# Optimization experiments

Hardware: AMD Instinct MI355X
Metric: run time of the kernel (lower is better)

## Reference

```python
import jax, jax.numpy as jnp
import numpy as np

B, T, I, H, O = 64, 1024, 64, 512, 64


def setup_inputs() -> dict:
    key = jax.random.key(0)
    ks = jax.random.split(key, 8)
    s = 1.0 / np.sqrt(H)  # PyTorch nn.RNN / nn.Linear init scale
    u = lambda k, shape: jax.random.uniform(k, shape, jnp.float32, -s, s)
    return {
        "x": jax.random.normal(ks[0], (B, T, I), jnp.float32),
        "h": jnp.zeros((1, B, H), jnp.float32),
        "W_ih": u(ks[1], (H, I)),
        "W_hh": u(ks[2], (H, H)),
        "b_ih": u(ks[3], (H,)),
        "b_hh": u(ks[4], (H,)),
        "W_out": u(ks[5], (O, H)),
        "b_out": u(ks[6], (O,)),
    }


def reference(x, h, W_ih, W_hh, b_ih, b_hh, W_out, b_out):
    # Precompute input projection for all timesteps: [B, T, H]
    xp = jnp.einsum('bti,hi->bth', x, W_ih) + b_ih + b_hh

    def step(h_prev, xp_t):
        # h_t = tanh(x_t W_ih^T + b_ih + h_{t-1} W_hh^T + b_hh)
        h_t = jnp.tanh(xp_t + h_prev @ W_hh.T)
        return h_t, h_t

    h0 = h[0]  # [B, H]
    h_last, hs = jax.lax.scan(step, h0, jnp.swapaxes(xp, 0, 1))  # hs: [T, B, H]
    hs = jnp.swapaxes(hs, 0, 1)  # [B, T, H]
    out = jnp.tanh(jnp.einsum('bth,oh->bto', hs, W_out) + b_out)  # [B, T, O]
    return out, h_last[None]  # h returned as [1, B, H]
```

## Files before the change

### kernel.cpp

```cpp
#include <hip/hip_runtime.h>
#include <cstdint>
#include <cstddef>


#define BB 64
#define TT 1024
#define II 64
#define HH 512
#define OO 64

__device__ __forceinline__ float tanh_fast(float v) {
  float e = exp2f(fabsf(v) * 2.8853900817779268f);
  float r = 1.0f - 2.0f * __builtin_amdgcn_rcpf(e + 1.0f);
  return copysignf(r, v);
}

__global__ __launch_bounds__(512, 1) void rnn_persist(
    const float* __restrict__ x, const float* __restrict__ h0,
    const float* __restrict__ Wih, const float* __restrict__ Whh,
    const float* __restrict__ bih, const float* __restrict__ bhh,
    const float* __restrict__ Wout, const float* __restrict__ bout,
    float* __restrict__ out, unsigned long long* __restrict__ ring) {
  const int tid = threadIdx.x;
  const int b   = blockIdx.x & 63;
  const int q   = blockIdx.x >> 6;
  const int n   = tid >> 2;
  const int q4  = tid & 3;
  const int row = q * 128 + n;

  __shared__ float h2[2][4][132];
  __shared__ float x2[2][II];

  float wh[128];
#pragma unroll
  for (int j = 0; j < 32; ++j) {
    const float4 v = *(const float4*)(Whh + (size_t)row * HH + q4 * 128 + j * 4);
    wh[4*j+0] = v.x; wh[4*j+1] = v.y; wh[4*j+2] = v.z; wh[4*j+3] = v.w;
  }
  float wi[16];
#pragma unroll
  for (int j = 0; j < 4; ++j) {
    const float4 v = *(const float4*)(Wih + (size_t)row * II + q4 * 16 + j * 4);
    wi[4*j+0] = v.x; wi[4*j+1] = v.y; wi[4*j+2] = v.z; wi[4*j+3] = v.w;
  }
  const float bias_n = bih[row] + bhh[row];

  const int l     = tid & 63;
  const int oc    = l & 15;
  const int o_loc = (tid >> 6) * 4 + (l >> 4);
  float wo[32];
  float bo = 0.0f;
  if (tid < 256) {
    const int o = q * 16 + o_loc;
#pragma unroll
    for (int j = 0; j < 32; ++j) wo[j] = Wout[(size_t)o * HH + oc + 16 * j];
    bo = bout[o];
  }

  const float* xb           = x + (size_t)b * TT * II;
  unsigned long long* ringb = ring + (size_t)b * 2 * HH;
  float* outb               = out + (size_t)b * TT * OO;

  for (int t = 1; t <= TT + 1; ++t) {
    const int hs = (t - 1) & 1;

    if (t <= TT && tid >= 256 && tid < 272) {
      const int j = tid - 256;
      const float4 v = *(const float4*)(xb + (size_t)(t - 1) * II + j * 4);
      *(float4*)&x2[t & 1][j * 4] = v;
    }

    if (tid < 256) {
      const int w  = tid >> 6;
      const int e0 = tid * 2;
      if (t == 1) {
        const float2 hv = *(const float2*)(h0 + (size_t)b * HH + e0);
        h2[0][w][e0 & 127]       = hv.x;
        h2[0][w][(e0 & 127) + 1] = hv.y;
      } else if (w != q) {
        const unsigned tgt = (unsigned)(t - 1);
        const unsigned long long* p0 = ringb + (size_t)hs * HH + e0;
        unsigned long long v0 = __hip_atomic_load(p0,     __ATOMIC_RELAXED, __HIP_MEMORY_SCOPE_AGENT);
        unsigned long long v1 = __hip_atomic_load(p0 + 1, __ATOMIC_RELAXED, __HIP_MEMORY_SCOPE_AGENT);
        bool d0 = ((unsigned)(v0 >> 32) == tgt);
        bool d1 = ((unsigned)(v1 >> 32) == tgt);
        while (!(d0 && d1)) {
          __builtin_amdgcn_s_sleep(8);
          if (!d0) {
            unsigned long long tv = __hip_atomic_load(p0,     __ATOMIC_RELAXED, __HIP_MEMORY_SCOPE_AGENT);
            if ((unsigned)(tv >> 32) == tgt) { v0 = tv; d0 = true; }
          }
          if (!d1) {
            unsigned long long tv = __hip_atomic_load(p0 + 1, __ATOMIC_RELAXED, __HIP_MEMORY_SCOPE_AGENT);
            if ((unsigned)(tv >> 32) == tgt) { v1 = tv; d1 = true; }
          }
        }
        h2[hs][w][e0 & 127]       = __uint_as_float((unsigned)v0);
        h2[hs][w][(e0 & 127) + 1] = __uint_as_float((unsigned)v1);
      }
    }
    __syncthreads();

    if (t <= TT) {
      const float* hp = &h2[hs][q4][0];
      float a0 = 0.f, a1 = 0.f, a2 = 0.f, a3 = 0.f;
#pragma unroll
      for (int j = 0; j < 128; j += 4) {
        a0 = fmaf(wh[j+0], hp[j+0], a0);
        a1 = fmaf(wh[j+1], hp[j+1], a1);
        a2 = fmaf(wh[j+2], hp[j+2], a2);
        a3 = fmaf(wh[j+3], hp[j+3], a3);
      }
      float ax = 0.f;
      const float* xp = &x2[t & 1][q4 * 16];
#pragma unroll
      for (int j = 0; j < 16; ++j) ax = fmaf(wi[j], xp[j], ax);

      float a = (a0 + a1) + (a2 + a3) + ax;
      a += __shfl_xor(a, 1);
      a += __shfl_xor(a, 2);
      if (q4 == 0) {
        const float hnew = tanh_fast(a + bias_n);
        h2[t & 1][q][n] = hnew;
        __hip_atomic_store(ringb + (size_t)(t & 1) * HH + row,
                           ((unsigned long long)(unsigned)t << 32) |
                               __float_as_uint(hnew),
                           __ATOMIC_RELAXED, __HIP_MEMORY_SCOPE_AGENT);
      }
    }

    if (t >= 2 && tid < 256) {
      float s0 = 0.f, s1 = 0.f;
#pragma unroll
      for (int j = 0; j < 32; j += 2) {
        s0 = fmaf(wo[j+0], h2[hs][(j+0) >> 3][oc + 16 * ((j+0) & 7)], s0);
        s1 = fmaf(wo[j+1], h2[hs][(j+1) >> 3][oc + 16 * ((j+1) & 7)], s1);
      }
      float s = s0 + s1;
      s += __shfl_xor(s, 1);
      s += __shfl_xor(s, 2);
      s += __shfl_xor(s, 4);
      s += __shfl_xor(s, 8);
      if (oc == 0) {
        outb[(size_t)(t - 2) * OO + q * 16 + o_loc] = tanh_fast(s + bo);
      }
    }

    if (t == TT + 1 && q == 0 && tid < 256) {
      const int e0 = tid * 2;
      float* hout = out + (size_t)BB * TT * OO + (size_t)b * HH + e0;
      hout[0] = h2[hs][e0 >> 7][e0 & 127];
      hout[1] = h2[hs][e0 >> 7][(e0 & 127) + 1];
    }
  }
}

extern "C" void kernel_launch(void* const* d_in, const int* in_sizes, int n_in,
                              void* d_out, int out_size, void* d_ws, size_t ws_size,
                              hipStream_t stream) {
  (void)in_sizes; (void)n_in; (void)out_size; (void)ws_size;
  const float* x    = (const float*)d_in[0];
  const float* h0   = (const float*)d_in[1];
  const float* Wih  = (const float*)d_in[2];
  const float* Whh  = (const float*)d_in[3];
  const float* bih  = (const float*)d_in[4];
  const float* bhh  = (const float*)d_in[5];
  const float* Wout = (const float*)d_in[6];
  const float* bout = (const float*)d_in[7];
  float* out = (float*)d_out;

  unsigned long long* ring = (unsigned long long*)d_ws;

  hipMemsetAsync(d_ws, 0, (size_t)BB * 2 * HH * 8, stream);

  rnn_persist<<<dim3(256), dim3(512), 0, stream>>>(
      x, h0, Wih, Whh, bih, bhh, Wout, bout, out, ring);
}
```

Measured before the change: 4.682 ms.

## Pack hidden-state pairs as bf16 in ring slots and prefetch x one step ahead

Cross-block hidden-state exchange now packs two neighbouring h values as bf16 into one 64-bit flagged slot. Each reader thread polls one slot instead of two, using 192 threads and no sleep in the spin loop. The x input for the next timestep is loaded into a register before the barrier and written to shared memory after it, hiding its global latency. This halves the ring traffic and polling work on the serial critical path. The cost is that the hidden state seen by other blocks is rounded to bf16, which adds error that builds up over the recurrence.

```diff
diff --git a/kernel.cpp b/kernel.cpp
--- a/kernel.cpp
+++ b/kernel.cpp
@@ -13,6 +13,14 @@
   float e = exp2f(fabsf(v) * 2.8853900817779268f);
   float r = 1.0f - 2.0f * __builtin_amdgcn_rcpf(e + 1.0f);
   return copysignf(r, v);
+}
+
+__device__ __forceinline__ unsigned f2bf(float f) {
+  unsigned u = __float_as_uint(f);
+  return (u + 0x7fffu + ((u >> 16) & 1u)) >> 16;
+}
+__device__ __forceinline__ float bf2f(unsigned b) {
+  return __uint_as_float(b << 16);
 }
 
 __global__ __launch_bounds__(512, 1) void rnn_persist(
@@ -58,48 +66,50 @@
   }
 
   const float* xb           = x + (size_t)b * TT * II;
-  unsigned long long* ringb = ring + (size_t)b * 2 * HH;
+  unsigned long long* ringb = ring + (size_t)b * 2 * 256;
   float* outb               = out + (size_t)b * TT * OO;
+
+  const bool xloader = (tid >= 256 && tid < 272);
+  if (xloader) {
+    const int j = tid - 256;
+    *(float4*)&x2[1][j * 4] = *(const float4*)(xb + j * 4);
+  }
 
   for (int t = 1; t <= TT + 1; ++t) {
     const int hs = (t - 1) & 1;
 
-    if (t <= TT && tid >= 256 && tid < 272) {
-      const int j = tid - 256;
-      const float4 v = *(const float4*)(xb + (size_t)(t - 1) * II + j * 4);
-      *(float4*)&x2[t & 1][j * 4] = v;
+    float4 xv;
+    if (t < TT && xloader) {
+      xv = *(const float4*)(xb + (size_t)t * II + (tid - 256) * 4);
     }
 
-    if (tid < 256) {
-      const int w  = tid >> 6;
-      const int e0 = tid * 2;
-      if (t == 1) {
+    if (t == 1) {
+      if (tid < 256) {
+        const int e0 = tid * 2;
         const float2 hv = *(const float2*)(h0 + (size_t)b * HH + e0);
-        h2[0][w][e0 & 127]       = hv.x;
-        h2[0][w][(e0 & 127) + 1] = hv.y;
-      } else if (w != q) {
-        const unsigned tgt = (unsigned)(t - 1);
-        const unsigned long long* p0 = ringb + (size_t)hs * HH + e0;
-        unsigned long long v0 = __hip_atomic_load(p0,     __ATOMIC_RELAXED, __HIP_MEMORY_SCOPE_AGENT);
-        unsigned long long v1 = __hip_atomic_load(p0 + 1, __ATOMIC_RELAXED, __HIP_MEMORY_SCOPE_AGENT);
-        bool d0 = ((unsigned)(v0 >> 32) == tgt);
-        bool d1 = ((unsigned)(v1 >> 32) == tgt);
-        while (!(d0 && d1)) {
-          __builtin_amdgcn_s_sleep(8);
-          if (!d0) {
-            unsigned long long tv = __hip_atomic_load(p0,     __ATOMIC_RELAXED, __HIP_MEMORY_SCOPE_AGENT);
-            if ((unsigned)(tv >> 32) == tgt) { v0 = tv; d0 = true; }
-          }
-          if (!d1) {
-            unsigned long long tv = __hip_atomic_load(p0 + 1, __ATOMIC_RELAXED, __HIP_MEMORY_SCOPE_AGENT);
-            if ((unsigned)(tv >> 32) == tgt) { v1 = tv; d1 = true; }
-          }
-        }
-        h2[hs][w][e0 & 127]       = __uint_as_float((unsigned)v0);
-        h2[hs][w][(e0 & 127) + 1] = __uint_as_float((unsigned)v1);
+        h2[0][tid >> 6][e0 & 127]       = hv.x;
+        h2[0][tid >> 6][(e0 & 127) + 1] = hv.y;
       }
+    } else if (tid < 192) {
+      const int wq = tid >> 6;
+      const int w  = wq + (wq >= q);
+      const int m  = tid & 63;
+      const unsigned tgt = (unsigned)(t - 1);
+      const unsigned long long* p = ringb + (size_t)hs * 256 + w * 64 + m;
+      unsigned long long v =
+          __hip_atomic_load(p, __ATOMIC_RELAXED, __HIP_MEMORY_SCOPE_AGENT);
+      while ((unsigned)(v >> 32) != tgt) {
+        v = __hip_atomic_load(p, __ATOMIC_RELAXED, __HIP_MEMORY_SCOPE_AGENT);
+      }
+      const unsigned lo = (unsigned)v & 0xffffu;
+      const unsigned hi = ((unsigned)v >> 16) & 0xffffu;
+      *(float2*)&h2[hs][w][2 * m] = make_float2(bf2f(lo), bf2f(hi));
     }
     __syncthreads();
+
+    if (t < TT && xloader) {
+      *(float4*)&x2[(t + 1) & 1][(tid - 256) * 4] = xv;
+    }
 
     if (t <= TT) {
       const float* hp = &h2[hs][q4][0];
@@ -119,13 +129,17 @@
       float a = (a0 + a1) + (a2 + a3) + ax;
       a += __shfl_xor(a, 1);
       a += __shfl_xor(a, 2);
+      const float hnew = tanh_fast(a + bias_n);
+      const float pv   = __shfl_xor(hnew, 4);
       if (q4 == 0) {
-        const float hnew = tanh_fast(a + bias_n);
         h2[t & 1][q][n] = hnew;
-        __hip_atomic_store(ringb + (size_t)(t & 1) * HH + row,
-                           ((unsigned long long)(unsigned)t << 32) |
-                               __float_as_uint(hnew),
-                           __ATOMIC_RELAXED, __HIP_MEMORY_SCOPE_AGENT);
+        if ((n & 1) == 0) {
+          const unsigned packed = f2bf(hnew) | (f2bf(pv) << 16);
+          __hip_atomic_store(
+              ringb + (size_t)(t & 1) * 256 + q * 64 + (n >> 1),
+              ((unsigned long long)(unsigned)t << 32) | packed,
+              __ATOMIC_RELAXED, __HIP_MEMORY_SCOPE_AGENT);
+        }
       }
     }
 
@@ -171,7 +185,7 @@
 
   unsigned long long* ring = (unsigned long long*)d_ws;
 
-  hipMemsetAsync(d_ws, 0, (size_t)BB * 2 * HH * 8, stream);
+  hipMemsetAsync(d_ws, 0, (size_t)BB * 2 * 256 * 8, stream);
 
   rnn_persist<<<dim3(256), dim3(512), 0, stream>>>(
       x, h0, Wih, Whh, bih, bhh, Wout, bout, out, ring);
```

After: 4.303 ms. -8.1%, faster.
